# Performance work log

Hardware: AMD Instinct MI355X
Metric: run time of the kernel (lower is better)

The kernel has to match this reference:

```python
import jax, jax.numpy as jnp
import numpy as np

NUM_HEADS = 16
D_KV = 64
NUM_BUCKETS = 32
MAX_DISTANCE = 128
LN_EPS = 1e-6


def _relative_position_bucket(seq_len):
    # bidirectional T5 bucketing
    ctx = jnp.arange(seq_len)[:, None]
    mem = jnp.arange(seq_len)[None, :]
    rel = mem - ctx  # [S, S]
    nb = NUM_BUCKETS // 2
    buckets = (rel > 0).astype(jnp.int32) * nb
    rel_abs = jnp.abs(rel)
    max_exact = nb // 2
    is_small = rel_abs < max_exact
    large = max_exact + (
        jnp.log(jnp.maximum(rel_abs, 1).astype(jnp.float32) / max_exact)
        / np.log(MAX_DISTANCE / max_exact)
        * (nb - max_exact)
    ).astype(jnp.int32)
    large = jnp.minimum(large, nb - 1)
    buckets = buckets + jnp.where(is_small, rel_abs, large)
    return buckets  # [S, S] int32


def setup_inputs() -> dict:
    key = jax.random.key(0)
    ks = jax.random.split(key, 6)
    B, S, D = 2, 2048, 1024
    scale = 1.0 / np.sqrt(D)
    return {
        "hidden_states": jax.random.normal(ks[0], (B, S, D), jnp.float32),
        "ln_weight": jnp.ones((D,), jnp.float32),
        "wq": jax.random.normal(ks[1], (D, NUM_HEADS * D_KV), jnp.float32) * scale,
        "wk": jax.random.normal(ks[2], (D, NUM_HEADS * D_KV), jnp.float32) * scale,
        "wv": jax.random.normal(ks[3], (D, NUM_HEADS * D_KV), jnp.float32) * scale,
        "wo": jax.random.normal(ks[4], (NUM_HEADS * D_KV, D), jnp.float32) * scale,
        "rel_bias": jax.random.normal(ks[5], (NUM_BUCKETS, NUM_HEADS), jnp.float32) * 0.1,
    }


def reference(hidden_states, ln_weight, wq, wk, wv, wo, rel_bias):
    B, S, D = hidden_states.shape
    # T5LayerNorm: RMS norm (no mean subtraction, no bias)
    var = jnp.mean(jnp.square(hidden_states), axis=-1, keepdims=True)
    normed = hidden_states * jax.lax.rsqrt(var + LN_EPS) * ln_weight

    def proj(w):
        return (normed @ w).reshape(B, S, NUM_HEADS, D_KV).transpose(0, 2, 1, 3)

    q = proj(wq)  # [B, H, S, dk]
    k = proj(wk)
    v = proj(wv)

    # T5 does NOT scale by sqrt(d_kv)
    scores = jnp.einsum("bhqd,bhkd->bhqk", q, k)

    buckets = _relative_position_bucket(S)           # [S, S]
    pos_bias = rel_bias[buckets]                     # [S, S, H]
    pos_bias = pos_bias.transpose(2, 0, 1)[None]     # [1, H, S, S]
    scores = scores + pos_bias

    attn = jax.nn.softmax(scores, axis=-1)
    ctx = jnp.einsum("bhqk,bhkd->bhqd", attn, v)
    ctx = ctx.transpose(0, 2, 1, 3).reshape(B, S, NUM_HEADS * D_KV)
    attn_out = ctx @ wo

    # dropout in eval mode -> identity; residual add
    return hidden_states + attn_out
```

## Files before the change

kernel.cpp:

```cpp
#include <hip/hip_runtime.h>

using s4     = __attribute__((ext_vector_type(4))) short;
using s8     = __attribute__((ext_vector_type(8))) short;
using f32x4  = __attribute__((ext_vector_type(4))) float;
using f32x4u = __attribute__((ext_vector_type(4), aligned(4))) float;

__device__ __forceinline__ float bf2f(short u) {
    union { unsigned int i; float f; } c;
    c.i = ((unsigned int)(unsigned short)u) << 16;
    return c.f;
}
__device__ __forceinline__ short f2bf(float f) {
    union { float f; unsigned int i; } c; c.f = f;
    unsigned int x = c.i;
    x += 0x7fffu + ((x >> 16) & 1u);
    return (short)(x >> 16);
}
__device__ __forceinline__ unsigned int cvt_pk_bf16(float lo, float hi) {
    unsigned int r;
    asm("v_cvt_pk_bf16_f32 %0, %1, %2" : "=v"(r) : "v"(lo), "v"(hi));
    return r;
}
__device__ __forceinline__ void gload16(const short* g, const char* lds) {
    __builtin_amdgcn_global_load_lds(
        (const __attribute__((address_space(1))) unsigned int*)(unsigned long long)(const void*)g,
        (__attribute__((address_space(3))) unsigned int*)(unsigned int)(unsigned long long)(const void*)lds,
        16, 0, 0);
}

#define MFMA(a, b, c) __builtin_amdgcn_mfma_f32_16x16x32_bf16(a, b, c, 0, 0, 0)
#define LOG2E 1.4426950408889634f

__global__ __launch_bounds__(256) void convT4_kernel(const float* __restrict__ w0,
                                                     const float* __restrict__ w1,
                                                     const float* __restrict__ w2,
                                                     const float* __restrict__ w3,
                                                     short* __restrict__ oqkv,
                                                     short* __restrict__ owo) {
    __shared__ float t[64][65];
    int z = blockIdx.z;
    const float* in = (z == 0) ? w0 : (z == 1) ? w1 : (z == 2) ? w2 : w3;
    short* out = (z < 3) ? (oqkv + (size_t)z * 1048576) : owo;
    int n0 = blockIdx.x * 64, k0 = blockIdx.y * 64;
    int tx = threadIdx.x & 15, ty = threadIdx.x >> 4;
#pragma unroll
    for (int i = 0; i < 4; ++i) {
        int r = ty + i * 16;
        f32x4 v = *(const f32x4*)(in + (size_t)(k0 + r) * 1024 + n0 + tx * 4);
        t[r][tx * 4 + 0] = v[0]; t[r][tx * 4 + 1] = v[1];
        t[r][tx * 4 + 2] = v[2]; t[r][tx * 4 + 3] = v[3];
    }
    __syncthreads();
#pragma unroll
    for (int i = 0; i < 4; ++i) {
        int r = ty + i * 16;
        s4 o;
#pragma unroll
        for (int e = 0; e < 4; ++e) o[e] = f2bf(t[tx * 4 + e][r]);
        *(s4*)(out + (size_t)(n0 + r) * 1024 + k0 + tx * 4) = o;
    }
}

__global__ __launch_bounds__(256) void rmsnorm_kernel(const float* __restrict__ x,
                                                      const float* __restrict__ w,
                                                      short* __restrict__ out) {
    int row = blockIdx.x;
    int tid = threadIdx.x;
    const float* xr = x + ((size_t)row << 10);
    f32x4 v = *(const f32x4*)(xr + tid * 4);
    float ss = v[0] * v[0] + v[1] * v[1] + v[2] * v[2] + v[3] * v[3];
#pragma unroll
    for (int off = 32; off > 0; off >>= 1) ss += __shfl_down(ss, off);
    __shared__ float red[4];
    if ((tid & 63) == 0) red[tid >> 6] = ss;
    __syncthreads();
    float total = red[0] + red[1] + red[2] + red[3];
    float r = rsqrtf(total * (1.0f / 1024.0f) + 1e-6f);
    f32x4 wv = *(const f32x4*)(w + tid * 4);
    s4 o;
    o[0] = f2bf(v[0] * r * wv[0]);
    o[1] = f2bf(v[1] * r * wv[1]);
    o[2] = f2bf(v[2] * r * wv[2]);
    o[3] = f2bf(v[3] * r * wv[3]);
    *(s4*)(out + ((size_t)row << 10) + tid * 4) = o;
}

__global__ void bias_table_kernel(const float* __restrict__ rel_bias, float* __restrict__ table) {
    int idx = blockIdx.x * 256 + threadIdx.x;
    if (idx >= 4095) return;
    int rel = 2047 - idx;
    int bucket = (rel > 0) ? 16 : 0;
    int a = (rel < 0) ? -rel : rel;
    if (a < 8) {
        bucket += a;
    } else {
        float l = logf((float)a * 0.125f) / 2.772588722239781f * 8.0f;
        int large = 8 + (int)l;
        bucket += (large > 15) ? 15 : large;
    }
#pragma unroll
    for (int h = 0; h < 16; ++h)
        table[h * 4095 + idx] = rel_bias[bucket * 16 + h] * LOG2E;
}

template<int BN, int WROWS, int WCOLS, int MODE>
__global__ __launch_bounds__(256) void gemm2(const short* __restrict__ A,
                                             const short* __restrict__ Bt,
                                             short* __restrict__ oq,
                                             short* __restrict__ ok,
                                             short* __restrict__ ov,
                                             float* __restrict__ Cf,
                                             const float* __restrict__ resid) {
    constexpr int MI = 128 / WROWS / 16;
    constexpr int NI = BN / WCOLS / 16;
    constexpr int NA = 4;
    constexpr int NB = BN / 32;
    const int K = 1024;
    __shared__ __align__(16) char lds[(128 + BN) * 128];
    char* A_base = lds;
    char* B_base = lds + 128 * 128;

    int nbx = gridDim.x;
    int nwg = nbx * gridDim.y;
    int lid = blockIdx.y * nbx + blockIdx.x;
    int nid = (lid & 7) * (nwg >> 3) + (lid >> 3);
    int m0 = (nid / nbx) << 7, n0 = (nid % nbx) * BN;

    int tid = threadIdx.x;
    int w = tid >> 6, l = tid & 63;
    int lr = l & 15, lg = l >> 4;
    int wm = (w / WCOLS) * (128 / WROWS);
    int wn = (w % WCOLS) * (BN / WCOLS);
    int sr = l >> 3;
    int cs = (l & 7) ^ sr;

    f32x4 acc[MI][NI] = {};

    for (int kk = 0; kk < K; kk += 64) {
        __syncthreads();
#pragma unroll
        for (int i = 0; i < NA; ++i) {
            int r = (w * NA + i) * 8 + sr;
            gload16(A + (size_t)(m0 + r) * K + kk + cs * 8, A_base + (w * NA + i) * 1024);
        }
#pragma unroll
        for (int i = 0; i < NB; ++i) {
            int r = (w * NB + i) * 8 + sr;
            gload16(Bt + (size_t)(n0 + r) * K + kk + cs * 8, B_base + (w * NB + i) * 1024);
        }
        __syncthreads();

        s8 af[2][MI], bfv[2][NI];
#pragma unroll
        for (int ks = 0; ks < 2; ++ks) {
            int chunk = ((ks * 4 + lg) ^ (lr & 7)) << 4;
#pragma unroll
            for (int mi = 0; mi < MI; ++mi)
                af[ks][mi] = *(const s8*)(A_base + (wm + mi * 16 + lr) * 128 + chunk);
#pragma unroll
            for (int ni = 0; ni < NI; ++ni)
                bfv[ks][ni] = *(const s8*)(B_base + (wn + ni * 16 + lr) * 128 + chunk);
        }
#pragma unroll
        for (int ks = 0; ks < 2; ++ks)
#pragma unroll
            for (int mi = 0; mi < MI; ++mi)
#pragma unroll
                for (int ni = 0; ni < NI; ++ni)
                    acc[mi][ni] = MFMA(af[ks][mi], bfv[ks][ni], acc[mi][ni]);
    }

#pragma unroll
    for (int mi = 0; mi < MI; ++mi) {
#pragma unroll
        for (int ni = 0; ni < NI; ++ni) {
#pragma unroll
            for (int j = 0; j < 4; ++j) {
                int r = m0 + wm + mi * 16 + lg * 4 + j;
                int c = n0 + wn + ni * 16 + lr;
                float v = acc[mi][ni][j];
                if (MODE == 0) {
                    size_t idx = ((size_t)r << 10) + c;
                    Cf[idx] = v + resid[idx];
                } else {
                    int b = r >> 11, sdx = r & 2047;
                    int which = c >> 10, nn = c & 1023;
                    int h = nn >> 6, d = nn & 63;
                    if (which == 0)
                        oq[(((size_t)(b * 16 + h) << 11) + sdx) * 64 + d] = f2bf(v * LOG2E);
                    else if (which == 1)
                        ok[(((size_t)(b * 16 + h) << 11) + sdx) * 64 + d] = f2bf(v);
                    else
                        ov[((size_t)((b * 16 + h) * 64 + d) << 11) + sdx] = f2bf(v);
                }
            }
        }
    }
}

__global__ __launch_bounds__(256) void attn_kernel(const short* __restrict__ Q,
                                                   const short* __restrict__ Km,
                                                   const short* __restrict__ VT,
                                                   const float* __restrict__ tabR,
                                                   short* __restrict__ ctx) {
    const int S = 2048;
    int bid = blockIdx.x;
    int qt = bid >> 5;
    int bh = ((bid & 7) << 2) | ((bid >> 3) & 3);
    int b = bh >> 4, h = bh & 15;
    const short* Qp = Q  + (size_t)bh * S * 64;
    const short* Kp = Km + (size_t)bh * S * 64;
    const short* Vp = VT + (size_t)bh * 64 * S;
    const float* tb0 = tabR + h * 4095;

    __shared__ __align__(16) short K_lds[64 * 64];
    __shared__ __align__(16) short V_lds[64 * 64];
    __shared__ __align__(16) short P_lds[4][16 * 64];

    int tid = threadIdx.x;
    int wave = tid >> 6, lane = tid & 63;
    int lr = lane & 15, lg = lane >> 4;
    int q0 = qt * 64 + wave * 16;

    const short* qrow = Qp + (size_t)(q0 + lr) * 64 + lg * 8;
    s8 qf0 = *(const s8*)(qrow);
    s8 qf1 = *(const s8*)(qrow + 32);

    s8 ones;
#pragma unroll
    for (int e = 0; e < 8; ++e) ones[e] = (short)0x3F80;

    f32x4 o_acc[4] = {};
    f32x4 o_l = {};
    float m_run = -1e30f;

    int k_row = tid >> 2;
    int kc0 = (tid & 3) * 2;
    char* k_wr0 = (char*)K_lds + k_row * 128 + ((kc0 ^ (k_row & 7)) << 4);
    char* k_wr1 = (char*)K_lds + k_row * 128 + (((kc0 + 1) ^ (k_row & 7)) << 4);
    char* v_wr0 = (char*)V_lds + k_row * 128 + ((kc0 ^ (k_row & 7)) << 4);
    char* v_wr1 = (char*)V_lds + k_row * 128 + (((kc0 + 1) ^ (k_row & 7)) << 4);

    const short* kp = Kp + (size_t)k_row * 64 + (tid & 3) * 16;
    s8 kv0 = *(const s8*)kp, kv1 = *(const s8*)(kp + 8);
    const short* vp = Vp + (size_t)k_row * S + (tid & 3) * 16;
    s8 vv0 = *(const s8*)vp, vv1 = *(const s8*)(vp + 8);

    char* pbase = (char*)P_lds + wave * 2048 + lr * 128;
    int psw = lr & 7;
    const float* tbl = tb0 + (q0 + lr - lg * 4 + 2044);

    const char* kr_base = (const char*)K_lds + lr * 128;
    int kch0 = (lg ^ (lr & 7)) << 4;
    int kch1 = ((4 + lg) ^ (lr & 7)) << 4;

    for (int kt0 = 0; kt0 < S; kt0 += 64) {
        __syncthreads();
        *(s8*)k_wr0 = kv0;
        *(s8*)k_wr1 = kv1;
        *(s8*)v_wr0 = vv0;
        *(s8*)v_wr1 = vv1;
        int nt = (kt0 + 64 < S) ? kt0 + 64 : kt0;
        kv0 = *(const s8*)(kp + (size_t)nt * 64);
        kv1 = *(const s8*)(kp + (size_t)nt * 64 + 8);
        vv0 = *(const s8*)(vp + nt);
        vv1 = *(const s8*)(vp + nt + 8);
        __syncthreads();

        f32x4 sc[4];
        __builtin_amdgcn_s_setprio(1);
#pragma unroll
        for (int kt = 0; kt < 4; ++kt) {
            s8 kf0 = *(const s8*)(kr_base + kt * 2048 + kch0);
            s8 kf1 = *(const s8*)(kr_base + kt * 2048 + kch1);
            f32x4 s = {};
            s = MFMA(kf0, qf0, s);
            s = MFMA(kf1, qf1, s);
            sc[kt] = s;
        }
        __builtin_amdgcn_s_setprio(0);

#pragma unroll
        for (int kt = 0; kt < 4; ++kt) {
            f32x4u bv = *(const f32x4u*)(tbl - kt0 - kt * 16);
#pragma unroll
            for (int j = 0; j < 4; ++j) sc[kt][j] += bv[3 - j];
        }

        float m0a = fmaxf(fmaxf(sc[0][0], sc[0][1]), fmaxf(sc[0][2], sc[0][3]));
        float m1a = fmaxf(fmaxf(sc[1][0], sc[1][1]), fmaxf(sc[1][2], sc[1][3]));
        float m2a = fmaxf(fmaxf(sc[2][0], sc[2][1]), fmaxf(sc[2][2], sc[2][3]));
        float m3a = fmaxf(fmaxf(sc[3][0], sc[3][1]), fmaxf(sc[3][2], sc[3][3]));
        float mt = fmaxf(fmaxf(m0a, m1a), fmaxf(m2a, m3a));
        mt = fmaxf(mt, __shfl_xor(mt, 16));
        mt = fmaxf(mt, __shfl_xor(mt, 32));

        if (__any(mt > m_run + 11.0f)) {
            float mn = fmaxf(m_run, mt);
            float scale = exp2f(m_run - mn);
            m_run = mn;
#pragma unroll
            for (int j = 0; j < 4; ++j) o_l[j] *= scale;
#pragma unroll
            for (int dt = 0; dt < 4; ++dt)
#pragma unroll
                for (int j = 0; j < 4; ++j) o_acc[dt][j] *= scale;
        }

#pragma unroll
        for (int kt = 0; kt < 4; ++kt) {
#pragma unroll
            for (int j = 0; j < 4; ++j) sc[kt][j] = exp2f(sc[kt][j] - m_run);
            uint2 pv;
            pv.x = cvt_pk_bf16(sc[kt][0], sc[kt][1]);
            pv.y = cvt_pk_bf16(sc[kt][2], sc[kt][3]);
            int sw = ((kt * 2 + (lg >> 1)) ^ psw) << 4;
            *(uint2*)(pbase + sw + (lg & 1) * 8) = pv;
        }

        s8 pf0 = *(const s8*)(pbase + ((lg ^ psw) << 4));
        s8 pf1 = *(const s8*)(pbase + (((4 + lg) ^ psw) << 4));
        __builtin_amdgcn_s_setprio(1);
#pragma unroll
        for (int dt = 0; dt < 4; ++dt) {
            int d = dt * 16 + lr;
            const char* vb = (const char*)V_lds + d * 128;
            s8 vf0 = *(const s8*)(vb + ((lg ^ (lr & 7)) << 4));
            s8 vf1 = *(const s8*)(vb + (((4 + lg) ^ (lr & 7)) << 4));
            o_acc[dt] = MFMA(vf0, pf0, o_acc[dt]);
            o_acc[dt] = MFMA(vf1, pf1, o_acc[dt]);
        }
        o_l = MFMA(ones, pf0, o_l);
        o_l = MFMA(ones, pf1, o_l);
        __builtin_amdgcn_s_setprio(0);
    }

    float rl = 1.0f / o_l[0];

    short* cbase = ctx + ((size_t)(b * 2048 + q0 + lr) << 10) + h * 64 + lg * 4;
#pragma unroll
    for (int dt = 0; dt < 4; ++dt) {
        uint2 o;
        o.x = cvt_pk_bf16(o_acc[dt][0] * rl, o_acc[dt][1] * rl);
        o.y = cvt_pk_bf16(o_acc[dt][2] * rl, o_acc[dt][3] * rl);
        *(uint2*)(cbase + dt * 16) = o;
    }
}

extern "C" void kernel_launch(void* const* d_in, const int* in_sizes, int n_in,
                              void* d_out, int out_size, void* d_ws, size_t ws_size,
                              hipStream_t stream) {
    const float* hidden = (const float*)d_in[0];
    const float* ln_w   = (const float*)d_in[1];
    const float* wq     = (const float*)d_in[2];
    const float* wk     = (const float*)d_in[3];
    const float* wv     = (const float*)d_in[4];
    const float* wo     = (const float*)d_in[5];
    const float* relb   = (const float*)d_in[6];
    float* out = (float*)d_out;

    char* ws = (char*)d_ws;
    const size_t SZ  = 8388608;
    const size_t WSZ = 2097152;
    short* normed = (short*)(ws);
    short* q      = (short*)(ws + SZ);
    short* k      = (short*)(ws + 2 * SZ);
    short* vt     = (short*)(ws + 3 * SZ);
    short* ctx    = (short*)(ws + 4 * SZ);
    short* wqkv_t = (short*)(ws + 5 * SZ);
    short* wo_t   = (short*)(ws + 5 * SZ + 3 * WSZ);
    float* table  = (float*)(ws + 5 * SZ + 4 * WSZ);

    convT4_kernel<<<dim3(16, 16, 4), 256, 0, stream>>>(wq, wk, wv, wo, wqkv_t, wo_t);
    rmsnorm_kernel<<<4096, 256, 0, stream>>>(hidden, ln_w, normed);
    bias_table_kernel<<<16, 256, 0, stream>>>(relb, table);
    gemm2<128, 2, 2, 1><<<dim3(24, 32), 256, 0, stream>>>(normed, wqkv_t, q, k, vt, nullptr, nullptr);
    attn_kernel<<<1024, 256, 0, stream>>>(q, k, vt, table, ctx);
    gemm2<128, 2, 2, 0><<<dim3(8, 32), 256, 0, stream>>>(ctx, wo_t, nullptr, nullptr, nullptr, out, hidden);
}
```

Before: 247.2 us.

## Process two query tiles per wave in attention and retile output GEMM

Each attention wave now handles two 16-row query tiles that share every K/V tile staged in LDS, halving the number of blocks and the K/V load and barrier cost per query. Scores, online softmax state and outputs are duplicated for both tiles, with MFMAs interleaved. The output projection GEMM switches to a smaller tile configuration with a larger grid. This raises register pressure, which may reduce occupancy, and leaves fewer attention blocks to spread across CUs.

```diff
diff --git a/kernel.cpp b/kernel.cpp
--- a/kernel.cpp
+++ b/kernel.cpp
@@ -215,24 +215,25 @@
 
     __shared__ __align__(16) short K_lds[64 * 64];
     __shared__ __align__(16) short V_lds[64 * 64];
-    __shared__ __align__(16) short P_lds[4][16 * 64];
+    __shared__ __align__(16) short P_lds[4 * 2 * 16 * 64];
 
     int tid = threadIdx.x;
     int wave = tid >> 6, lane = tid & 63;
     int lr = lane & 15, lg = lane >> 4;
-    int q0 = qt * 64 + wave * 16;
-
-    const short* qrow = Qp + (size_t)(q0 + lr) * 64 + lg * 8;
-    s8 qf0 = *(const s8*)(qrow);
-    s8 qf1 = *(const s8*)(qrow + 32);
+    int q0 = qt * 128 + wave * 16;
+
+    const short* qrowA = Qp + (size_t)(q0 + lr) * 64 + lg * 8;
+    const short* qrowB = qrowA + 64 * 64;
+    s8 qfA0 = *(const s8*)(qrowA),      qfA1 = *(const s8*)(qrowA + 32);
+    s8 qfB0 = *(const s8*)(qrowB),      qfB1 = *(const s8*)(qrowB + 32);
 
     s8 ones;
 #pragma unroll
     for (int e = 0; e < 8; ++e) ones[e] = (short)0x3F80;
 
-    f32x4 o_acc[4] = {};
-    f32x4 o_l = {};
-    float m_run = -1e30f;
+    f32x4 oA[4] = {}, oB[4] = {};
+    f32x4 lA = {}, lB = {};
+    float mA = -1e30f, mB = -1e30f;
 
     int k_row = tid >> 2;
     int kc0 = (tid & 3) * 2;
@@ -246,9 +247,11 @@
     const short* vp = Vp + (size_t)k_row * S + (tid & 3) * 16;
     s8 vv0 = *(const s8*)vp, vv1 = *(const s8*)(vp + 8);
 
-    char* pbase = (char*)P_lds + wave * 2048 + lr * 128;
+    char* pbA = (char*)P_lds + wave * 4096 + lr * 128;
+    char* pbB = pbA + 2048;
     int psw = lr & 7;
-    const float* tbl = tb0 + (q0 + lr - lg * 4 + 2044);
+    const float* tblA = tb0 + (q0 + lr - lg * 4 + 2044);
+    const float* tblB = tblA + 64;
 
     const char* kr_base = (const char*)K_lds + lr * 128;
     int kch0 = (lg ^ (lr & 7)) << 4;
@@ -267,59 +270,87 @@
         vv1 = *(const s8*)(vp + nt + 8);
         __syncthreads();
 
-        f32x4 sc[4];
+        f32x4u bvA[4], bvB[4];
+#pragma unroll
+        for (int kt = 0; kt < 4; ++kt) {
+            bvA[kt] = *(const f32x4u*)(tblA - kt0 - kt * 16);
+            bvB[kt] = *(const f32x4u*)(tblB - kt0 - kt * 16);
+        }
+
+        f32x4 scA[4], scB[4];
         __builtin_amdgcn_s_setprio(1);
 #pragma unroll
         for (int kt = 0; kt < 4; ++kt) {
             s8 kf0 = *(const s8*)(kr_base + kt * 2048 + kch0);
             s8 kf1 = *(const s8*)(kr_base + kt * 2048 + kch1);
-            f32x4 s = {};
-            s = MFMA(kf0, qf0, s);
-            s = MFMA(kf1, qf1, s);
-            sc[kt] = s;
+            f32x4 sa = {}, sb = {};
+            sa = MFMA(kf0, qfA0, sa);
+            sb = MFMA(kf0, qfB0, sb);
+            sa = MFMA(kf1, qfA1, sa);
+            sb = MFMA(kf1, qfB1, sb);
+            scA[kt] = sa;
+            scB[kt] = sb;
         }
         __builtin_amdgcn_s_setprio(0);
 
 #pragma unroll
+        for (int kt = 0; kt < 4; ++kt)
+#pragma unroll
+            for (int j = 0; j < 4; ++j) {
+                scA[kt][j] += bvA[kt][3 - j];
+                scB[kt][j] += bvB[kt][3 - j];
+            }
+
+        float t0A = fmaxf(fmaxf(scA[0][0], scA[0][1]), fmaxf(scA[0][2], scA[0][3]));
+        float t1A = fmaxf(fmaxf(scA[1][0], scA[1][1]), fmaxf(scA[1][2], scA[1][3]));
+        float t2A = fmaxf(fmaxf(scA[2][0], scA[2][1]), fmaxf(scA[2][2], scA[2][3]));
+        float t3A = fmaxf(fmaxf(scA[3][0], scA[3][1]), fmaxf(scA[3][2], scA[3][3]));
+        float mtA = fmaxf(fmaxf(t0A, t1A), fmaxf(t2A, t3A));
+        float t0B = fmaxf(fmaxf(scB[0][0], scB[0][1]), fmaxf(scB[0][2], scB[0][3]));
+        float t1B = fmaxf(fmaxf(scB[1][0], scB[1][1]), fmaxf(scB[1][2], scB[1][3]));
+        float t2B = fmaxf(fmaxf(scB[2][0], scB[2][1]), fmaxf(scB[2][2], scB[2][3]));
+        float t3B = fmaxf(fmaxf(scB[3][0], scB[3][1]), fmaxf(scB[3][2], scB[3][3]));
+        float mtB = fmaxf(fmaxf(t0B, t1B), fmaxf(t2B, t3B));
+        mtA = fmaxf(mtA, __shfl_xor(mtA, 16));
+        mtB = fmaxf(mtB, __shfl_xor(mtB, 16));
+        mtA = fmaxf(mtA, __shfl_xor(mtA, 32));
+        mtB = fmaxf(mtB, __shfl_xor(mtB, 32));
+
+        if (__any((mtA > mA + 11.0f) || (mtB > mB + 11.0f))) {
+            float mnA = fmaxf(mA, mtA);
+            float mnB = fmaxf(mB, mtB);
+            float sA = exp2f(mA - mnA);
+            float sB = exp2f(mB - mnB);
+            mA = mnA; mB = mnB;
+#pragma unroll
+            for (int j = 0; j < 4; ++j) { lA[j] *= sA; lB[j] *= sB; }
+#pragma unroll
+            for (int dt = 0; dt < 4; ++dt)
+#pragma unroll
+                for (int j = 0; j < 4; ++j) { oA[dt][j] *= sA; oB[dt][j] *= sB; }
+        }
+
+#pragma unroll
         for (int kt = 0; kt < 4; ++kt) {
-            f32x4u bv = *(const f32x4u*)(tbl - kt0 - kt * 16);
-#pragma unroll
-            for (int j = 0; j < 4; ++j) sc[kt][j] += bv[3 - j];
-        }
-
-        float m0a = fmaxf(fmaxf(sc[0][0], sc[0][1]), fmaxf(sc[0][2], sc[0][3]));
-        float m1a = fmaxf(fmaxf(sc[1][0], sc[1][1]), fmaxf(sc[1][2], sc[1][3]));
-        float m2a = fmaxf(fmaxf(sc[2][0], sc[2][1]), fmaxf(sc[2][2], sc[2][3]));
-        float m3a = fmaxf(fmaxf(sc[3][0], sc[3][1]), fmaxf(sc[3][2], sc[3][3]));
-        float mt = fmaxf(fmaxf(m0a, m1a), fmaxf(m2a, m3a));
-        mt = fmaxf(mt, __shfl_xor(mt, 16));
-        mt = fmaxf(mt, __shfl_xor(mt, 32));
-
-        if (__any(mt > m_run + 11.0f)) {
-            float mn = fmaxf(m_run, mt);
-            float scale = exp2f(m_run - mn);
-            m_run = mn;
-#pragma unroll
-            for (int j = 0; j < 4; ++j) o_l[j] *= scale;
-#pragma unroll
-            for (int dt = 0; dt < 4; ++dt)
-#pragma unroll
-                for (int j = 0; j < 4; ++j) o_acc[dt][j] *= scale;
-        }
-
-#pragma unroll
-        for (int kt = 0; kt < 4; ++kt) {
-#pragma unroll
-            for (int j = 0; j < 4; ++j) sc[kt][j] = exp2f(sc[kt][j] - m_run);
-            uint2 pv;
-            pv.x = cvt_pk_bf16(sc[kt][0], sc[kt][1]);
-            pv.y = cvt_pk_bf16(sc[kt][2], sc[kt][3]);
+#pragma unroll
+            for (int j = 0; j < 4; ++j) {
+                scA[kt][j] = exp2f(scA[kt][j] - mA);
+                scB[kt][j] = exp2f(scB[kt][j] - mB);
+            }
             int sw = ((kt * 2 + (lg >> 1)) ^ psw) << 4;
-            *(uint2*)(pbase + sw + (lg & 1) * 8) = pv;
-        }
-
-        s8 pf0 = *(const s8*)(pbase + ((lg ^ psw) << 4));
-        s8 pf1 = *(const s8*)(pbase + (((4 + lg) ^ psw) << 4));
+            uint2 pva, pvb;
+            pva.x = cvt_pk_bf16(scA[kt][0], scA[kt][1]);
+            pva.y = cvt_pk_bf16(scA[kt][2], scA[kt][3]);
+            pvb.x = cvt_pk_bf16(scB[kt][0], scB[kt][1]);
+            pvb.y = cvt_pk_bf16(scB[kt][2], scB[kt][3]);
+            *(uint2*)(pbA + sw + (lg & 1) * 8) = pva;
+            *(uint2*)(pbB + sw + (lg & 1) * 8) = pvb;
+        }
+
+        s8 pfA0 = *(const s8*)(pbA + ((lg ^ psw) << 4));
+        s8 pfA1 = *(const s8*)(pbA + (((4 + lg) ^ psw) << 4));
+        s8 pfB0 = *(const s8*)(pbB + ((lg ^ psw) << 4));
+        s8 pfB1 = *(const s8*)(pbB + (((4 + lg) ^ psw) << 4));
         __builtin_amdgcn_s_setprio(1);
 #pragma unroll
         for (int dt = 0; dt < 4; ++dt) {
@@ -327,23 +358,32 @@
             const char* vb = (const char*)V_lds + d * 128;
             s8 vf0 = *(const s8*)(vb + ((lg ^ (lr & 7)) << 4));
             s8 vf1 = *(const s8*)(vb + (((4 + lg) ^ (lr & 7)) << 4));
-            o_acc[dt] = MFMA(vf0, pf0, o_acc[dt]);
-            o_acc[dt] = MFMA(vf1, pf1, o_acc[dt]);
-        }
-        o_l = MFMA(ones, pf0, o_l);
-        o_l = MFMA(ones, pf1, o_l);
+            oA[dt] = MFMA(vf0, pfA0, oA[dt]);
+            oB[dt] = MFMA(vf0, pfB0, oB[dt]);
+            oA[dt] = MFMA(vf1, pfA1, oA[dt]);
+            oB[dt] = MFMA(vf1, pfB1, oB[dt]);
+        }
+        lA = MFMA(ones, pfA0, lA);
+        lA = MFMA(ones, pfA1, lA);
+        lB = MFMA(ones, pfB0, lB);
+        lB = MFMA(ones, pfB1, lB);
         __builtin_amdgcn_s_setprio(0);
     }
 
-    float rl = 1.0f / o_l[0];
-
-    short* cbase = ctx + ((size_t)(b * 2048 + q0 + lr) << 10) + h * 64 + lg * 4;
+    float rlA = 1.0f / lA[0];
+    float rlB = 1.0f / lB[0];
+
+    short* cbA = ctx + ((size_t)(b * 2048 + q0 + lr) << 10) + h * 64 + lg * 4;
+    short* cbB = cbA + (64 << 10);
 #pragma unroll
     for (int dt = 0; dt < 4; ++dt) {
-        uint2 o;
-        o.x = cvt_pk_bf16(o_acc[dt][0] * rl, o_acc[dt][1] * rl);
-        o.y = cvt_pk_bf16(o_acc[dt][2] * rl, o_acc[dt][3] * rl);
-        *(uint2*)(cbase + dt * 16) = o;
+        uint2 oa, ob;
+        oa.x = cvt_pk_bf16(oA[dt][0] * rlA, oA[dt][1] * rlA);
+        oa.y = cvt_pk_bf16(oA[dt][2] * rlA, oA[dt][3] * rlA);
+        ob.x = cvt_pk_bf16(oB[dt][0] * rlB, oB[dt][1] * rlB);
+        ob.y = cvt_pk_bf16(oB[dt][2] * rlB, oB[dt][3] * rlB);
+        *(uint2*)(cbA + dt * 16) = oa;
+        *(uint2*)(cbB + dt * 16) = ob;
     }
 }
 
@@ -375,6 +415,6 @@
     rmsnorm_kernel<<<4096, 256, 0, stream>>>(hidden, ln_w, normed);
     bias_table_kernel<<<16, 256, 0, stream>>>(relb, table);
     gemm2<128, 2, 2, 1><<<dim3(24, 32), 256, 0, stream>>>(normed, wqkv_t, q, k, vt, nullptr, nullptr);
-    attn_kernel<<<1024, 256, 0, stream>>>(q, k, vt, table, ctx);
-    gemm2<128, 2, 2, 0><<<dim3(8, 32), 256, 0, stream>>>(ctx, wo_t, nullptr, nullptr, nullptr, out, hidden);
-}
+    attn_kernel<<<512, 256, 0, stream>>>(q, k, vt, table, ctx);
+    gemm2<64, 4, 1, 0><<<dim3(16, 32), 256, 0, stream>>>(ctx, wo_t, nullptr, nullptr, nullptr, out, hidden);
+}
```

New measurement: 243.2 us. About the same (-1.6%).
